# Kernel tuning notes

Hardware: AMD Instinct MI355X
Metric: run time of the kernel (lower is better)

Reference implementation:

```python
import jax, jax.numpy as jnp
import numpy as np

TAU = 0.07          # softmax temperature
THR = 0.3           # Jaccard similarity threshold for positive pairs
EPS_NORM = 1e-12    # F.normalize eps


def setup_inputs() -> dict:
    key = jax.random.key(0)
    k1, k2, k3 = jax.random.split(key, 3)
    N, D, A = 4096, 128, 512
    z1 = jax.random.normal(k1, (N, D), dtype=jnp.float32)
    z2 = jax.random.normal(k2, (N, D), dtype=jnp.float32)
    labels = jax.random.randint(k3, (N, A), 0, 2).astype(jnp.int32)
    return {"z1": z1, "z2": z2, "labels": labels}


def _l2_normalize(x):
    n = jnp.linalg.norm(x, axis=-1, keepdims=True)
    return x / jnp.maximum(n, EPS_NORM)


def reference(z1, z2, labels):
    # Implements the N > 1000 (chunked) branch of SupConLoss.forward,
    # vectorized over all anchors at once (chunking is just tiling; math identical).
    N = z1.shape[0]
    idx = jnp.arange(N)

    z1n = _l2_normalize(z1)                       # (N, D)
    z2n = _l2_normalize(z2)                       # (N, D)
    z_all = jnp.concatenate([z1n, z2n], axis=0)   # (2N, D)

    # Jaccard label similarity -> positive-pair mask
    lab = labels.astype(jnp.float32)              # (N, A)
    inter = lab @ lab.T                           # (N, N)
    s = lab.sum(axis=1, keepdims=True)            # (N, 1)
    union = s + s.T - inter
    jaccard = inter / (union + 1e-8)
    pos_label = jaccard >= THR                    # (N, N) bool

    # pos mask over 2N columns: label-positives in both halves,
    # augmented view [j, N+j] forced True, self column [j, j] forced False.
    pos_mask = jnp.concatenate([pos_label, pos_label], axis=1)  # (N, 2N)
    pos_mask = pos_mask.at[idx, N + idx].set(True)
    pos_mask = pos_mask.at[idx, idx].set(False)

    # similarity of z1 anchors against all 2N embeddings
    sim = (z1n @ z_all.T) / TAU                   # (N, 2N)
    sim = sim - jax.lax.stop_gradient(sim.max(axis=1, keepdims=True))
    exp_sim = jnp.exp(sim)

    # denominator excludes the self column [j, j]
    denom = exp_sim.sum(axis=1, keepdims=True) - exp_sim[idx, idx][:, None]
    log_prob = sim - jnp.log(denom + 1e-8)

    num_pos = jnp.maximum(pos_mask.sum(axis=1), 1)
    loss_per_sample = -jnp.where(pos_mask, log_prob, 0.0).sum(axis=1) / num_pos
    return loss_per_sample.sum() / N
```

## Files before the change

kernel.cpp:

```cpp
#include <hip/hip_runtime.h>
#include <math.h>

#define N_ROWS 4096
#define DIM    128
#define A_LAB  512
#define INV_TAU 14.285714285714286f
#define C_EXP   20.609929155556620f

typedef __attribute__((ext_vector_type(8))) short short8;
typedef __attribute__((ext_vector_type(4))) float f32x4;
typedef __attribute__((ext_vector_type(4))) int i32x4;
typedef __attribute__((ext_vector_type(16))) int i32x16;


__device__ __forceinline__ unsigned short f2bf(float f) {
  unsigned int u = __builtin_bit_cast(unsigned int, f);
  u += 0x7fffu + ((u >> 16) & 1u);
  return (unsigned short)(u >> 16);
}

__global__ __launch_bounds__(256) void k_norm_pack(
    const float* __restrict__ z1, const float* __restrict__ z2,
    const int* __restrict__ labels,
    unsigned int* __restrict__ zbf, uint2* __restrict__ labs8,
    int* __restrict__ s, float* __restrict__ part, float* __restrict__ out)
{
  {
    const int idx = blockIdx.x * 256 + threadIdx.x;
    if (idx < 3 * 4096) part[idx] = 0.0f;
    if (idx == 0) out[0] = 0.0f;
  }
  const int wave = threadIdx.x >> 6, lane = threadIdx.x & 63;
  const int r = blockIdx.x * 4 + wave;
  const float* src = (r < N_ROWS) ? (z1 + (size_t)r * DIM)
                                  : (z2 + (size_t)(r - N_ROWS) * DIM);
  float2 x = ((const float2*)src)[lane];
  float ss = x.x * x.x + x.y * x.y;
  #pragma unroll
  for (int off = 32; off > 0; off >>= 1) ss += __shfl_xor(ss, off);
  const float inv = 1.0f / fmaxf(sqrtf(ss), 1e-12f);
  const unsigned int lo = f2bf(x.x * inv);
  const unsigned int hi = f2bf(x.y * inv);
  {
    const int u = lane >> 2, p = lane & 3;
    const int kf = u >> 2, quad = u & 3;
    const int g = r >> 4;
    zbf[(size_t)(((g * 4 + kf) * 64) + ((r & 15) + (quad << 4))) * 4 + p] = (hi << 16) | lo;
  }

  if (r < N_ROWS) {
    const int4* lp = (const int4*)(labels + (size_t)r * A_LAB);
    const int4 a = lp[2 * lane], b = lp[2 * lane + 1];
    const unsigned int w0 = (unsigned int)(a.x != 0)       | ((unsigned int)(a.y != 0) << 8)
                          | ((unsigned int)(a.z != 0) << 16) | ((unsigned int)(a.w != 0) << 24);
    const unsigned int w1 = (unsigned int)(b.x != 0)       | ((unsigned int)(b.y != 0) << 8)
                          | ((unsigned int)(b.z != 0) << 16) | ((unsigned int)(b.w != 0) << 24);
    uint2 v; v.x = w0; v.y = w1;
    const int ul = lane >> 1, hp = lane & 1;
    const int ks = ul >> 1, h = ul & 1;
    const int g = r >> 5;
    labs8[(size_t)(((g * 16 + ks) * 64) + ((r & 31) + (h << 5))) * 2 + hp] = v;
    int cnt = __popc(w0) + __popc(w1);
    #pragma unroll
    for (int off = 32; off > 0; off >>= 1) cnt += __shfl_xor(cnt, off);
    if (lane == 0) s[r] = cnt;
  }
}

__global__ __launch_bounds__(512, 4) void k_fused(
    const unsigned char* __restrict__ labs8, const int* __restrict__ s,
    const unsigned short* __restrict__ zbf, float* __restrict__ part)
{
  __shared__ unsigned int pmL[128 * 4];
  const int tid = threadIdx.x;
  const int ibase = blockIdx.x * 128, jbase = blockIdx.y * 128;
  const int wave = tid >> 6, lane = tid & 63;
  const bool diag = (ibase == jbase);
  const char* gl = (const char*)labs8;
  const char* gz = (const char*)zbf;

  const int jwr = (wave >> 2) * 64;
  const int jwc = (wave & 3) * 32;
  const int col32 = lane & 31, h = lane >> 5;

  const int s3i = 3 * s[ibase + jwr + lane];
  const int s3j = 3 * s[jbase + jwc + col32];

  i32x16 jacc[2];
  #pragma unroll
  for (int rt = 0; rt < 2; ++rt)
    #pragma unroll
    for (int e = 0; e < 16; ++e) jacc[rt][e] = 0;

  const int gI = (ibase + jwr) >> 5;
  const int gJ = (jbase + jwc) >> 5;
  #pragma unroll
  for (int ks = 0; ks < 16; ++ks) {
    i32x4 a[2], b;
    #pragma unroll
    for (int rt = 0; rt < 2; ++rt)
      a[rt] = *(const i32x4*)(gl + (size_t)(((gI + rt) * 16 + ks) * 64 + lane) * 16);
    b = *(const i32x4*)(gl + (size_t)((gJ * 16 + ks) * 64 + lane) * 16);
    #pragma unroll
    for (int rt = 0; rt < 2; ++rt)
      jacc[rt] = __builtin_amdgcn_mfma_i32_32x32x32_i8(a[rt], b, jacc[rt], 0, 0, 0);
  }

  const int wl = wave & 3;
  #pragma unroll
  for (int rt = 0; rt < 2; ++rt)
    #pragma unroll
    for (int reg = 0; reg < 16; ++reg) {
      const int r0 = (reg & 3) + 8 * (reg >> 2);
      const int si = __shfl(s3i, rt * 32 + r0 + 4 * h);
      const bool pred = 13 * jacc[rt][reg] >= si + s3j;
      const unsigned long long bal = __ballot(pred);
      const int lr = jwr + rt * 32 + r0;
      if (lane == 0)      pmL[lr * 4 + wl]       = (unsigned int)bal;
      else if (lane == 1) pmL[(lr + 4) * 4 + wl] = (unsigned int)(bal >> 32);
    }

  const int col = lane & 15, quad = lane >> 4;
  const int srow = wave * 16;
  const int gA = (ibase + srow) >> 4;
  short8 afr[4];
  #pragma unroll
  for (int kf = 0; kf < 4; ++kf)
    afr[kf] = *(const short8*)(gz + (size_t)((gA * 4 + kf) * 64 + lane) * 16);

  __syncthreads();

  uint4 pw[4];
  #pragma unroll
  for (int reg = 0; reg < 4; ++reg)
    pw[reg] = *(const uint4*)&pmL[(srow + quad * 4 + reg) * 4];

  float lacc[4], Sacc[4], Pcnt[4];
  #pragma unroll
  for (int reg = 0; reg < 4; ++reg) { lacc[reg] = 0; Sacc[reg] = 0; Pcnt[reg] = 0; }

  #pragma unroll
  for (int half = 0; half < 2; ++half) {
    const int gB = ((half ? N_ROWS : 0) + jbase) >> 4;
    f32x4 acc[8];
    #pragma unroll
    for (int nt = 0; nt < 8; ++nt) acc[nt] = (f32x4){0, 0, 0, 0};

    #pragma unroll
    for (int nt = 0; nt < 8; ++nt) {
      short8 bfr[4];
      #pragma unroll
      for (int kf = 0; kf < 4; ++kf)
        bfr[kf] = *(const short8*)(gz + (size_t)(((gB + nt) * 4 + kf) * 64 + lane) * 16);
      #pragma unroll
      for (int kf = 0; kf < 4; ++kf)
        acc[nt] = __builtin_amdgcn_mfma_f32_16x16x32_bf16(afr[kf], bfr[kf], acc[nt], 0, 0, 0);
    }

    if (!diag) {
      #pragma unroll
      for (int nt = 0; nt < 8; ++nt) {
        const int bitpos = (nt & 1) * 16 + col;
        #pragma unroll
        for (int reg = 0; reg < 4; ++reg) {
          const unsigned int w = ((const unsigned int*)&pw[reg])[nt >> 1];
          const float d = acc[nt][reg];
          lacc[reg] += exp2f(fmaf(d, C_EXP, -C_EXP));
          if ((w >> bitpos) & 1) Sacc[reg] += d;
        }
      }
    } else {
      const bool left = (half == 0);
      #pragma unroll
      for (int nt = 0; nt < 8; ++nt) {
        const int joff = nt * 16 + col;
        const int jc = jbase + joff;
        const int bitpos = joff & 31;
        #pragma unroll
        for (int reg = 0; reg < 4; ++reg) {
          const int i = ibase + srow + quad * 4 + reg;
          const unsigned int w = ((const unsigned int*)&pw[reg])[nt >> 1];
          const float d = acc[nt][reg];
          const bool bit = (w >> bitpos) & 1;
          const bool self = left && (jc == i);
          const bool pos = left ? (bit && !self) : (bit || (jc == i));
          const float e = exp2f(fmaf(d, C_EXP, -C_EXP));
          if (!self) lacc[reg] += e;
          if (pos) { Sacc[reg] += d; Pcnt[reg] += 1.0f; }
        }
      }
    }
  }

  #pragma unroll
  for (int reg = 0; reg < 4; ++reg) {
    float l = lacc[reg], S = Sacc[reg], P = Pcnt[reg];
    #pragma unroll
    for (int m = 1; m < 16; m <<= 1) {
      l += __shfl_xor(l, m);
      S += __shfl_xor(S, m);
      if (diag) P += __shfl_xor(P, m);
    }
    if (col == 0) {
      const int li = srow + quad * 4 + reg;
      const int i = ibase + li;
      if (!diag) {
        const uint4 w = pw[reg];
        P = 2.0f * (float)(__popc(w.x) + __popc(w.y) + __popc(w.z) + __popc(w.w));
      }
      atomicAdd(&part[i], l);
      atomicAdd(&part[4096 + i], S);
      atomicAdd(&part[8192 + i], P);
    }
  }
}

__global__ __launch_bounds__(128) void k_loss(
    const float* __restrict__ part, float* __restrict__ out)
{
  const int a = blockIdx.x * 128 + threadIdx.x;
  const float l = part[a];
  const float S = part[4096 + a];
  const float P = part[8192 + a];
  const float np = fmaxf(P, 1.0f);
  float v = INV_TAU + logf(l + 1e-8f) - (S * INV_TAU) / np;
  #pragma unroll
  for (int off = 32; off > 0; off >>= 1) v += __shfl_xor(v, off);
  __shared__ float ws2[2];
  const int wave = threadIdx.x >> 6, lane = threadIdx.x & 63;
  if (lane == 0) ws2[wave] = v;
  __syncthreads();
  if (threadIdx.x == 0) atomicAdd(out, (ws2[0] + ws2[1]) * (1.0f / (float)N_ROWS));
}

extern "C" void kernel_launch(void* const* d_in, const int* in_sizes, int n_in,
                              void* d_out, int out_size, void* d_ws, size_t ws_size,
                              hipStream_t stream) {
  const float* z1 = (const float*)d_in[0];
  const float* z2 = (const float*)d_in[1];
  const int* labels = (const int*)d_in[2];
  float* out = (float*)d_out;
  char* ws = (char*)d_ws;

  unsigned int* zbf    = (unsigned int*)(ws);
  uint2* labs8         = (uint2*)(ws + 2097152);
  int* s               = (int*)(ws + 4194304);
  float* part          = (float*)(ws + 4210688);

  hipLaunchKernelGGL(k_norm_pack, dim3(2048), dim3(256), 0, stream,
                     z1, z2, labels, zbf, labs8, s, part, out);
  hipLaunchKernelGGL(k_fused, dim3(32, 32), dim3(512), 0, stream,
                     (const unsigned char*)labs8, s, (const unsigned short*)zbf, part);
  hipLaunchKernelGGL(k_loss, dim3(32), dim3(128), 0, stream, part, out);
}
```

Before: 109.2 us.

## Exploit Jaccard mask symmetry: compute upper-triangle tiles and reuse transposed mask

Result: slower. 169.4 us (+55.1%).

```diff
diff --git a/kernel.cpp b/kernel.cpp
--- a/kernel.cpp
+++ b/kernel.cpp
@@ -57,9 +57,9 @@
                           | ((unsigned int)(b.z != 0) << 16) | ((unsigned int)(b.w != 0) << 24);
     uint2 v; v.x = w0; v.y = w1;
     const int ul = lane >> 1, hp = lane & 1;
-    const int ks = ul >> 1, h = ul & 1;
+    const int ks = ul >> 1, hh = ul & 1;
     const int g = r >> 5;
-    labs8[(size_t)(((g * 16 + ks) * 64) + ((r & 31) + (h << 5))) * 2 + hp] = v;
+    labs8[(size_t)(((g * 16 + ks) * 64) + ((r & 31) + (hh << 5))) * 2 + hp] = v;
     int cnt = __popc(w0) + __popc(w1);
     #pragma unroll
     for (int off = 32; off > 0; off >>= 1) cnt += __shfl_xor(cnt, off);
@@ -71,146 +71,197 @@
     const unsigned char* __restrict__ labs8, const int* __restrict__ s,
     const unsigned short* __restrict__ zbf, float* __restrict__ part)
 {
-  __shared__ unsigned int pmL[128 * 4];
+  __shared__ __align__(16) char panel[65536];
+  __shared__ __align__(16) unsigned int pmL[128 * 4];
+  __shared__ __align__(16) unsigned int pmT[128 * 4];
+
   const int tid = threadIdx.x;
-  const int ibase = blockIdx.x * 128, jbase = blockIdx.y * 128;
   const int wave = tid >> 6, lane = tid & 63;
-  const bool diag = (ibase == jbase);
-  const char* gl = (const char*)labs8;
-  const char* gz = (const char*)zbf;
+  const char* gl_ = (const char*)labs8;
+  const char* gz  = (const char*)zbf;
 
   const int jwr = (wave >> 2) * 64;
   const int jwc = (wave & 3) * 32;
   const int col32 = lane & 31, h = lane >> 5;
-
-  const int s3i = 3 * s[ibase + jwr + lane];
-  const int s3j = 3 * s[jbase + jwc + col32];
-
-  i32x16 jacc[2];
-  #pragma unroll
-  for (int rt = 0; rt < 2; ++rt)
-    #pragma unroll
-    for (int e = 0; e < 16; ++e) jacc[rt][e] = 0;
-
-  const int gI = (ibase + jwr) >> 5;
-  const int gJ = (jbase + jwc) >> 5;
-  #pragma unroll
-  for (int ks = 0; ks < 16; ++ks) {
-    i32x4 a[2], b;
-    #pragma unroll
-    for (int rt = 0; rt < 2; ++rt)
-      a[rt] = *(const i32x4*)(gl + (size_t)(((gI + rt) * 16 + ks) * 64 + lane) * 16);
-    b = *(const i32x4*)(gl + (size_t)((gJ * 16 + ks) * 64 + lane) * 16);
-    #pragma unroll
-    for (int rt = 0; rt < 2; ++rt)
-      jacc[rt] = __builtin_amdgcn_mfma_i32_32x32x32_i8(a[rt], b, jacc[rt], 0, 0, 0);
-  }
-
   const int wl = wave & 3;
-  #pragma unroll
-  for (int rt = 0; rt < 2; ++rt)
-    #pragma unroll
-    for (int reg = 0; reg < 16; ++reg) {
-      const int r0 = (reg & 3) + 8 * (reg >> 2);
-      const int si = __shfl(s3i, rt * 32 + r0 + 4 * h);
-      const bool pred = 13 * jacc[rt][reg] >= si + s3j;
-      const unsigned long long bal = __ballot(pred);
-      const int lr = jwr + rt * 32 + r0;
-      if (lane == 0)      pmL[lr * 4 + wl]       = (unsigned int)bal;
-      else if (lane == 1) pmL[(lr + 4) * 4 + wl] = (unsigned int)(bal >> 32);
-    }
-
   const int col = lane & 15, quad = lane >> 4;
   const int srow = wave * 16;
-  const int gA = (ibase + srow) >> 4;
-  short8 afr[4];
-  #pragma unroll
-  for (int kf = 0; kf < 4; ++kf)
-    afr[kf] = *(const short8*)(gz + (size_t)((gA * 4 + kf) * 64 + lane) * 16);
-
-  __syncthreads();
-
-  uint4 pw[4];
-  #pragma unroll
-  for (int reg = 0; reg < 4; ++reg)
-    pw[reg] = *(const uint4*)&pmL[(srow + quad * 4 + reg) * 4];
-
-  float lacc[4], Sacc[4], Pcnt[4];
-  #pragma unroll
-  for (int reg = 0; reg < 4; ++reg) { lacc[reg] = 0; Sacc[reg] = 0; Pcnt[reg] = 0; }
-
-  #pragma unroll
-  for (int half = 0; half < 2; ++half) {
-    const int gB = ((half ? N_ROWS : 0) + jbase) >> 4;
-    f32x4 acc[8];
-    #pragma unroll
-    for (int nt = 0; nt < 8; ++nt) acc[nt] = (f32x4){0, 0, 0, 0};
-
-    #pragma unroll
-    for (int nt = 0; nt < 8; ++nt) {
-      short8 bfr[4];
+
+  const int ntasks = (blockIdx.x < 496) ? 1 : 2;
+  for (int t = 0; t < ntasks; ++t) {
+    int bi, bj;
+    if (blockIdx.x < 496) {
+      int r = blockIdx.x, row = 0;
+      while (r >= 31 - row) { r -= 31 - row; ++row; }
+      bi = row; bj = row + 1 + r;
+    } else {
+      bi = bj = 2 * (blockIdx.x - 496) + t;
+    }
+    const int ibase = bi * 128, jbase = bj * 128;
+    const bool diag = (bi == bj);
+
+    __syncthreads();
+
+    const int gI0 = ibase >> 5;
+    #pragma unroll
+    for (int q = 0; q < 8; ++q) {
+      const int u = wave * 8 + q;
+      const uint4 v = *(const uint4*)(gl_ +
+          (size_t)(((gI0 + (u >> 4)) * 16 + (u & 15)) * 64 + lane) * 16);
+      *(uint4*)(panel + (size_t)u * 1024 + lane * 16) = v;
+    }
+    const int s3i = 3 * s[ibase + jwr + lane];
+    const int s3j = 3 * s[jbase + jwc + col32];
+
+    __syncthreads();
+
+    i32x16 jacc[2];
+    #pragma unroll
+    for (int rt = 0; rt < 2; ++rt)
+      #pragma unroll
+      for (int e = 0; e < 16; ++e) jacc[rt][e] = 0;
+
+    const int gJ = (jbase + jwc) >> 5;
+    #pragma unroll
+    for (int ks = 0; ks < 16; ++ks) {
+      i32x4 a[2], b;
+      #pragma unroll
+      for (int rt = 0; rt < 2; ++rt)
+        a[rt] = *(const i32x4*)(panel +
+            (size_t)((((wave >> 2) * 2 + rt) * 16 + ks) * 1024) + lane * 16);
+      b = *(const i32x4*)(gl_ + (size_t)((gJ * 16 + ks) * 64 + lane) * 16);
+      #pragma unroll
+      for (int rt = 0; rt < 2; ++rt)
+        jacc[rt] = __builtin_amdgcn_mfma_i32_32x32x32_i8(a[rt], b, jacc[rt], 0, 0, 0);
+    }
+
+    unsigned int tw0 = 0, tw1 = 0;
+    #pragma unroll
+    for (int rt = 0; rt < 2; ++rt)
+      #pragma unroll
+      for (int reg = 0; reg < 16; ++reg) {
+        const int r0 = (reg & 3) + 8 * (reg >> 2);
+        const int si = __shfl(s3i, rt * 32 + r0 + 4 * h);
+        const bool pred = 13 * jacc[rt][reg] >= si + s3j;
+        const unsigned long long bal = __ballot(pred);
+        const int lr = jwr + rt * 32 + r0;
+        if (lane == 0)      pmL[lr * 4 + wl]       = (unsigned int)bal;
+        else if (lane == 1) pmL[(lr + 4) * 4 + wl] = (unsigned int)(bal >> 32);
+        const unsigned int pb = ((unsigned int)pred) << (r0 + 4 * h);
+        if (rt == 0) tw0 |= pb; else tw1 |= pb;
+      }
+    tw0 |= __shfl_xor(tw0, 32);
+    tw1 |= __shfl_xor(tw1, 32);
+    if (h == 0) pmT[(jwc + col32) * 4 + (jwr >> 5)]     = tw0;
+    else        pmT[(jwc + col32) * 4 + (jwr >> 5) + 1] = tw1;
+
+    const int npass = diag ? 1 : 2;
+    for (int pass = 0; pass < npass; ++pass) {
+      const int abase = pass ? jbase : ibase;
+      const int cbase = pass ? ibase : jbase;
+
+      __syncthreads();
+
+      #pragma unroll
+      for (int q = 0; q < 8; ++q) {
+        const int u = wave * 8 + q;
+        const int kf = u & 3, hg = u >> 2;
+        const int gS = ((hg & 8) ? ((N_ROWS + cbase) >> 4) : (cbase >> 4)) + (hg & 7);
+        const uint4 v = *(const uint4*)(gz + (size_t)((gS * 4 + kf) * 64 + lane) * 16);
+        *(uint4*)(panel + (size_t)u * 1024 + lane * 16) = v;
+      }
+
+      const int gA = (abase + srow) >> 4;
+      short8 afr[4];
       #pragma unroll
       for (int kf = 0; kf < 4; ++kf)
-        bfr[kf] = *(const short8*)(gz + (size_t)(((gB + nt) * 4 + kf) * 64 + lane) * 16);
-      #pragma unroll
-      for (int kf = 0; kf < 4; ++kf)
-        acc[nt] = __builtin_amdgcn_mfma_f32_16x16x32_bf16(afr[kf], bfr[kf], acc[nt], 0, 0, 0);
-    }
-
-    if (!diag) {
-      #pragma unroll
-      for (int nt = 0; nt < 8; ++nt) {
-        const int bitpos = (nt & 1) * 16 + col;
+        afr[kf] = *(const short8*)(gz + (size_t)((gA * 4 + kf) * 64 + lane) * 16);
+
+      const unsigned int* pm = pass ? pmT : pmL;
+      uint4 pw[4];
+      #pragma unroll
+      for (int reg = 0; reg < 4; ++reg)
+        pw[reg] = *(const uint4*)&pm[(srow + quad * 4 + reg) * 4];
+
+      __syncthreads();
+
+      float lacc[4], Sacc[4], Pcnt[4];
+      #pragma unroll
+      for (int reg = 0; reg < 4; ++reg) { lacc[reg] = 0; Sacc[reg] = 0; Pcnt[reg] = 0; }
+
+      #pragma unroll
+      for (int half = 0; half < 2; ++half) {
+        f32x4 acc[8];
         #pragma unroll
-        for (int reg = 0; reg < 4; ++reg) {
-          const unsigned int w = ((const unsigned int*)&pw[reg])[nt >> 1];
-          const float d = acc[nt][reg];
-          lacc[reg] += exp2f(fmaf(d, C_EXP, -C_EXP));
-          if ((w >> bitpos) & 1) Sacc[reg] += d;
+        for (int nt = 0; nt < 8; ++nt) acc[nt] = (f32x4){0, 0, 0, 0};
+
+        #pragma unroll
+        for (int nt = 0; nt < 8; ++nt) {
+          short8 bfr[4];
+          #pragma unroll
+          for (int kf = 0; kf < 4; ++kf)
+            bfr[kf] = *(const short8*)(panel +
+                (size_t)(((half * 8 + nt) * 4 + kf) * 1024) + lane * 16);
+          #pragma unroll
+          for (int kf = 0; kf < 4; ++kf)
+            acc[nt] = __builtin_amdgcn_mfma_f32_16x16x32_bf16(afr[kf], bfr[kf], acc[nt], 0, 0, 0);
+        }
+
+        if (!diag) {
+          #pragma unroll
+          for (int nt = 0; nt < 8; ++nt) {
+            const int bitpos = (nt & 1) * 16 + col;
+            #pragma unroll
+            for (int reg = 0; reg < 4; ++reg) {
+              const unsigned int w = ((const unsigned int*)&pw[reg])[nt >> 1];
+              const float d = acc[nt][reg];
+              lacc[reg] += exp2f(fmaf(d, C_EXP, -C_EXP));
+              if ((w >> bitpos) & 1) Sacc[reg] += d;
+            }
+          }
+        } else {
+          const bool left = (half == 0);
+          #pragma unroll
+          for (int nt = 0; nt < 8; ++nt) {
+            const int joff = nt * 16 + col;
+            const int jc = cbase + joff;
+            const int bitpos = joff & 31;
+            #pragma unroll
+            for (int reg = 0; reg < 4; ++reg) {
+              const int i = abase + srow + quad * 4 + reg;
+              const unsigned int w = ((const unsigned int*)&pw[reg])[nt >> 1];
+              const float d = acc[nt][reg];
+              const bool bit = (w >> bitpos) & 1;
+              const bool self = left && (jc == i);
+              const bool pos = left ? (bit && !self) : (bit || (jc == i));
+              const float e = exp2f(fmaf(d, C_EXP, -C_EXP));
+              if (!self) lacc[reg] += e;
+              if (pos) { Sacc[reg] += d; Pcnt[reg] += 1.0f; }
+            }
+          }
         }
       }
-    } else {
-      const bool left = (half == 0);
-      #pragma unroll
-      for (int nt = 0; nt < 8; ++nt) {
-        const int joff = nt * 16 + col;
-        const int jc = jbase + joff;
-        const int bitpos = joff & 31;
+
+      #pragma unroll
+      for (int reg = 0; reg < 4; ++reg) {
+        float l = lacc[reg], S = Sacc[reg], P = Pcnt[reg];
         #pragma unroll
-        for (int reg = 0; reg < 4; ++reg) {
-          const int i = ibase + srow + quad * 4 + reg;
-          const unsigned int w = ((const unsigned int*)&pw[reg])[nt >> 1];
-          const float d = acc[nt][reg];
-          const bool bit = (w >> bitpos) & 1;
-          const bool self = left && (jc == i);
-          const bool pos = left ? (bit && !self) : (bit || (jc == i));
-          const float e = exp2f(fmaf(d, C_EXP, -C_EXP));
-          if (!self) lacc[reg] += e;
-          if (pos) { Sacc[reg] += d; Pcnt[reg] += 1.0f; }
+        for (int m = 1; m < 16; m <<= 1) {
+          l += __shfl_xor(l, m);
+          S += __shfl_xor(S, m);
+          if (diag) P += __shfl_xor(P, m);
+        }
+        if (col == 0) {
+          const int i = abase + srow + quad * 4 + reg;
+          if (!diag) {
+            const uint4 w = pw[reg];
+            P = 2.0f * (float)(__popc(w.x) + __popc(w.y) + __popc(w.z) + __popc(w.w));
+          }
+          atomicAdd(&part[i], l);
+          atomicAdd(&part[4096 + i], S);
+          atomicAdd(&part[8192 + i], P);
         }
       }
-    }
-  }
-
-  #pragma unroll
-  for (int reg = 0; reg < 4; ++reg) {
-    float l = lacc[reg], S = Sacc[reg], P = Pcnt[reg];
-    #pragma unroll
-    for (int m = 1; m < 16; m <<= 1) {
-      l += __shfl_xor(l, m);
-      S += __shfl_xor(S, m);
-      if (diag) P += __shfl_xor(P, m);
-    }
-    if (col == 0) {
-      const int li = srow + quad * 4 + reg;
-      const int i = ibase + li;
-      if (!diag) {
-        const uint4 w = pw[reg];
-        P = 2.0f * (float)(__popc(w.x) + __popc(w.y) + __popc(w.z) + __popc(w.w));
-      }
-      atomicAdd(&part[i], l);
-      atomicAdd(&part[4096 + i], S);
-      atomicAdd(&part[8192 + i], P);
     }
   }
 }
@@ -249,7 +300,7 @@
 
   hipLaunchKernelGGL(k_norm_pack, dim3(2048), dim3(256), 0, stream,
                      z1, z2, labels, zbf, labs8, s, part, out);
-  hipLaunchKernelGGL(k_fused, dim3(32, 32), dim3(512), 0, stream,
+  hipLaunchKernelGGL(k_fused, dim3(512), dim3(512), 0, stream,
                      (const unsigned char*)labs8, s, (const unsigned short*)zbf, part);
   hipLaunchKernelGGL(k_loss, dim3(32), dim3(128), 0, stream, part, out);
 }
```
